# Performance work log

Hardware: AMD Instinct MI355X
Metric: run time of the kernel (lower is better)

## Reference

```python
import jax, jax.numpy as jnp
import numpy as np

K = 3
KK = K * K
PAD = 1          # kernel_size // 2
MAX_SHIFT = 8.0  # bias_range > 0
DEG = 2          # degrees = (2, 2), paon_type 'a'


def setup_inputs() -> dict:
    key = jax.random.key(0)
    ks = jax.random.split(key, 6)
    B, C, O, H, W = 4, 64, 64, 160, 160
    x = jax.random.normal(ks[0], (B, C, H, W), jnp.float32)
    # offset conv is 1x1: weight [2*K*K, C], bias [2*K*K]
    off_w = jax.random.normal(ks[1], (2 * KK, C), jnp.float32) * 0.1
    off_b = jax.random.normal(ks[2], (2 * KK,), jnp.float32) * 0.1
    scale = 1.0 / np.sqrt(C * KK).astype(np.float32)
    w_m = jax.random.normal(ks[3], (DEG * O, C, K, K), jnp.float32) * scale
    w_n = jax.random.normal(ks[4], (DEG * O, C, K, K), jnp.float32) * scale
    w0 = jax.random.normal(ks[5], (O,), jnp.float32) * 0.1
    return {"x": x, "off_w": off_w, "off_b": off_b, "w_m": w_m, "w_n": w_n, "w0": w0}


def _bilinear_sample(x, py, px):
    """x: [B,C,H,W]; py,px: [B,KK,H,W] -> [B,C,KK,H,W]; zero outside bounds."""
    B, C, H, W = x.shape
    xf = x.reshape(B, C, H * W)
    y0 = jnp.floor(py)
    x0 = jnp.floor(px)
    wy = py - y0
    wx = px - x0
    y0i = y0.astype(jnp.int32)
    x0i = x0.astype(jnp.int32)
    out = jnp.zeros((B, C) + py.shape[1:], x.dtype)
    corners = ((0, 0, (1 - wy) * (1 - wx)), (0, 1, (1 - wy) * wx),
               (1, 0, wy * (1 - wx)), (1, 1, wy * wx))
    for dy, dx, wgt in corners:
        yy = y0i + dy
        xx = x0i + dx
        valid = (yy >= 0) & (yy < H) & (xx >= 0) & (xx < W)
        idx = jnp.clip(yy, 0, H - 1) * W + jnp.clip(xx, 0, W - 1)
        g = jax.vmap(lambda f, i: f[:, i])(xf, idx.reshape(B, -1))  # [B,C,KK*H*W]
        out = out + g.reshape(B, C, *py.shape[1:]) * (wgt * valid)[:, None]
    return out


def _after_poly_a(y, ch, o, take_abs):
    # channel reorder + groupwise sum, per PaLaBase.after_poly_a
    order = np.array([(k * ch) % (ch * o) + k // o for k in range(ch * o)])
    y = y[:, order].reshape(y.shape[0], ch, o, *y.shape[2:])
    return jnp.abs(y).sum(2) if take_abs else y.sum(2)


def reference(x, off_w, off_b, w_m, w_n, w0):
    B, C, H, W = x.shape
    O = w0.shape[0]
    # --- DeformOffset: 1x1 conv -> clamp to image -> tanh soft-limit ---
    off_r = jnp.einsum('bchw,oc->bohw', x, off_w) + off_b[None, :, None, None]
    gy = jnp.arange(H, dtype=x.dtype)[None, None, :, None]
    gx = jnp.arange(W, dtype=x.dtype)[None, None, None, :]
    oy = jnp.clip(off_r[:, 0::2], -gy, H - gy)  # [B,KK,H,W] (dy per kernel pos)
    ox = jnp.clip(off_r[:, 1::2], -gx, W - gx)  # [B,KK,H,W] (dx per kernel pos)
    soft = lambda o: jnp.where(jnp.abs(o) >= MAX_SHIFT,
                               MAX_SHIFT * jnp.tanh(o / MAX_SHIFT), o)
    oy, ox = soft(oy), soft(ox)
    # --- deformable sampling grid (stride=1, dilation=1, zero padding) ---
    kidx = jnp.arange(KK)
    kh = (kidx // K).astype(x.dtype)[None, :, None, None]
    kw = (kidx % K).astype(x.dtype)[None, :, None, None]
    base_y = (jnp.arange(H, dtype=x.dtype) - PAD)[None, None, :, None]
    base_x = (jnp.arange(W, dtype=x.dtype) - PAD)[None, None, None, :]
    py = base_y + kh + oy
    px = base_x + kw + ox
    samp = _bilinear_sample(x, py, px)  # [B,C,KK,H,W]
    # --- Pade numerator / denominator convs on the sampled tensor ---
    pm_raw = jnp.einsum('bckhw,ock->bohw', samp, w_m.reshape(DEG * O, C, KK))
    qn_raw = jnp.einsum('bckhw,ock->bohw', samp, w_n.reshape(DEG * O, C, KK))
    pm = _after_poly_a(pm_raw, O, DEG, take_abs=False)
    qn = _after_poly_a(qn_raw, O, DEG, take_abs=True)
    # prepare_for_div_a: (pm + w0, 1 + qn)
    return (pm + w0[None, :, None, None]) / (1.0 + qn)
```

## Files before the change

### kernel.cpp

```cpp
#include <hip/hip_runtime.h>
#include <hip/hip_bf16.h>
#include <hip/hip_fp16.h>

#define Hh 160
#define Ww 160
#define Cc 64
#define HWc 25600
#define Bb 4

typedef __attribute__((ext_vector_type(8))) short short8;
typedef __attribute__((ext_vector_type(4))) float f32x4;

__device__ __forceinline__ unsigned short f2bf(float f) {
  unsigned int u = __float_as_uint(f);
  unsigned int r = u + 0x7FFFu + ((u >> 16) & 1u);
  return (unsigned short)(r >> 16);
}
__device__ __forceinline__ float bflo(unsigned int u) {
  return __uint_as_float(u << 16);
}
__device__ __forceinline__ float bfhi(unsigned int u) {
  return __uint_as_float(u & 0xffff0000u);
}

__global__ __launch_bounds__(256) void k_prep(
    const float* __restrict__ x, const float* __restrict__ wm,
    const float* __restrict__ wn, const float* __restrict__ ow,
    unsigned short* __restrict__ xT, unsigned short* __restrict__ bf) {
  if (blockIdx.x < 1600) {
    __shared__ unsigned short s[64][65];
    int wg = blockIdx.x;
    int b = wg / 400;
    int pix0 = (wg % 400) * 64;
    int l = threadIdx.x & 63, wv = threadIdx.x >> 6;
    const float* xb = x + (size_t)b * Cc * HWc + pix0;
#pragma unroll
    for (int i = 0; i < 16; i++) {
      int c = i * 4 + wv;
      s[c][l] = f2bf(xb[(size_t)c * HWc + l]);
    }
    __syncthreads();
    int p = threadIdx.x >> 2, ck = threadIdx.x & 3;
    unsigned int w[8];
#pragma unroll
    for (int j = 0; j < 8; j++) {
      unsigned int a = s[ck * 16 + 2 * j][p];
      unsigned int bb = s[ck * 16 + 2 * j + 1][p];
      w[j] = a | (bb << 16);
    }
    unsigned short* dst = xT + ((size_t)(b * HWc + pix0 + p)) * 64 + ck * 16;
    ((uint4*)dst)[0] = make_uint4(w[0], w[1], w[2], w[3]);
    ((uint4*)dst)[1] = make_uint4(w[4], w[5], w[6], w[7]);
  } else {
    int i = (blockIdx.x - 1600) * 256 + threadIdx.x;
    if (i < 9 * 2 * 12 * 64 * 8) {
      int j2 = i & 7;
      int lane = (i >> 3) & 63;
      int ntck = i >> 9;
      int nt = ntck % 12;
      int ck = ntck / 12;
      int kk = ck >> 1;
      int chunk = ck & 1;
      int n = nt * 16 + (lane & 15);
      int c = chunk * 32 + (lane >> 4) * 8 + j2;
      float v;
      if (n < 64)
        v = wm[(n * 64 + c) * 9 + kk] + wm[((n + 64) * 64 + c) * 9 + kk];
      else
        v = wn[((n - 64) * 64 + c) * 9 + kk];
      bf[i] = f2bf(v);
    } else if (i < 9 * 2 * 12 * 64 * 8 + 2 * 2 * 64 * 8) {
      int j = i - 9 * 2 * 12 * 64 * 8;
      int j2 = j & 7;
      int lane = (j >> 3) & 63;
      int rest = j >> 9;
      int ntile = rest & 1;
      int chunk = rest >> 1;
      int n = ntile * 16 + (lane & 15);
      int c = chunk * 32 + (lane >> 4) * 8 + j2;
      bf[i] = (n < 18) ? f2bf(ow[n * 64 + c]) : (unsigned short)0;
    }
  }
}

__device__ __forceinline__ void gather2(const char* __restrict__ gbase, uint4 D,
                                        int chB, uint4& c00, uint4& c01,
                                        uint4& c10, uint4& c11, float& w00,
                                        float& w01, float& w10, float& w11) {
  int bb = D.x + chB;
  int dxB = (int)(D.y & 0xffffu);
  int dyB = (int)(D.y >> 16);
  c00 = *(const uint4*)(gbase + bb);
  c01 = *(const uint4*)(gbase + bb + dxB);
  c10 = *(const uint4*)(gbase + bb + dyB);
  c11 = *(const uint4*)(gbase + bb + (dxB + dyB));
  float2 wA = __half22float2(*(const __half2*)&D.z);
  float2 wB = __half22float2(*(const __half2*)&D.w);
  w00 = wA.x; w01 = wA.y; w10 = wB.x; w11 = wB.y;
}

__device__ __forceinline__ void combine_write(unsigned short* Arow,
                                              const uint4& c00, const uint4& c01,
                                              const uint4& c10, const uint4& c11,
                                              float w00, float w01, float w10,
                                              float w11) {
  const unsigned int* a = (const unsigned int*)&c00;
  const unsigned int* b = (const unsigned int*)&c01;
  const unsigned int* c = (const unsigned int*)&c10;
  const unsigned int* d = (const unsigned int*)&c11;
  unsigned int o[4];
#pragma unroll
  for (int j = 0; j < 4; j++) {
    float lo = bflo(a[j]) * w00 + bflo(b[j]) * w01 + bflo(c[j]) * w10 +
               bflo(d[j]) * w11;
    float hi = bfhi(a[j]) * w00 + bfhi(b[j]) * w01 + bfhi(c[j]) * w10 +
               bfhi(d[j]) * w11;
    __hip_bfloat162 hh = __float22bfloat162_rn(make_float2(lo, hi));
    o[j] = *(unsigned int*)&hh;
  }
  *(uint4*)Arow = make_uint4(o[0], o[1], o[2], o[3]);
}

__global__ __launch_bounds__(256) void k_main(
    const unsigned short* __restrict__ xT, const float* __restrict__ w0,
    const float* __restrict__ off_b, const unsigned short* __restrict__ bfrag,
    const unsigned short* __restrict__ obfrag, float* __restrict__ out) {
  __shared__ unsigned short A[2][64 * 72];
  __shared__ uint4 gdesc[576];
  float2* spy = (float2*)&A[0][0];
  const int tid = threadIdx.x;
  const int wg = blockIdx.x;
  const int band = wg & 7;
  const int local = wg >> 3;
  const int b = local / 50;
  const int pix0 = band * 3200 + (local % 50) * 64;
  const int wv = tid >> 6;
  const int l = tid & 63;
  const int lm = l & 15;
  const int quad = l >> 4;
  const int ch8 = l & 7;
  const int pr = l >> 3;
  const int chB = ch8 * 16;

  const unsigned short* xTb = xT + (size_t)b * HWc * 64;
  const char* gbase = (const char*)xTb;

  f32x4 acc[3][4];
  const f32x4 zero = {0.f, 0.f, 0.f, 0.f};
#pragma unroll
  for (int j = 0; j < 3; j++)
#pragma unroll
    for (int pt = 0; pt < 4; pt++) acc[j][pt] = zero;

  {
    f32x4 aO0 = zero, aO1 = zero;
    const unsigned short* xrow = xTb + (size_t)(pix0 + wv * 16 + lm) * 64;
#pragma unroll
    for (int chunk = 0; chunk < 2; chunk++) {
      short8 sb = *(const short8*)(xrow + chunk * 32 + quad * 8);
      short8 wf0 = *(const short8*)&obfrag[((chunk * 2 + 0) * 64 + l) * 8];
      short8 wf1 = *(const short8*)&obfrag[((chunk * 2 + 1) * 64 + l) * 8];
      aO0 = __builtin_amdgcn_mfma_f32_16x16x32_bf16(wf0, sb, aO0, 0, 0, 0);
      aO1 = __builtin_amdgcn_mfma_f32_16x16x32_bf16(wf1, sb, aO1, 0, 0, 0);
    }
    int pix = pix0 + wv * 16 + lm;
    int h = pix / Ww, w = pix % Ww;
    float fh = (float)h, fw = (float)w;
#pragma unroll
    for (int rr = 0; rr < 2; rr++) {
      int n = quad * 4 + 2 * rr;
      int kk = n >> 1;
      float oy = aO0[2 * rr] + off_b[n];
      float ox = aO0[2 * rr + 1] + off_b[n + 1];
      oy = fminf(fmaxf(oy, -fh), 160.0f - fh);
      ox = fminf(fmaxf(ox, -fw), 160.0f - fw);
      if (fabsf(oy) >= 8.0f) oy = 8.0f * tanhf(oy * 0.125f);
      if (fabsf(ox) >= 8.0f) ox = 8.0f * tanhf(ox * 0.125f);
      spy[kk * 64 + wv * 16 + lm] =
          make_float2(fh - 1.0f + (float)(kk / 3) + oy,
                      fw - 1.0f + (float)(kk % 3) + ox);
    }
    if (quad == 0) {
      float oy = aO1[0] + off_b[16];
      float ox = aO1[1] + off_b[17];
      oy = fminf(fmaxf(oy, -fh), 160.0f - fh);
      ox = fminf(fmaxf(ox, -fw), 160.0f - fw);
      if (fabsf(oy) >= 8.0f) oy = 8.0f * tanhf(oy * 0.125f);
      if (fabsf(ox) >= 8.0f) ox = 8.0f * tanhf(ox * 0.125f);
      spy[8 * 64 + wv * 16 + lm] =
          make_float2(fh + 1.0f + oy, fw + 1.0f + ox);
    }
  }
  __syncthreads();

  for (int e = tid; e < 576; e += 256) {
    float2 P = spy[e];
    float py = P.x, pxv = P.y;
    float y0f = floorf(py), x0f = floorf(pxv);
    float wy = py - y0f, wx = pxv - x0f;
    int y0 = (int)y0f, x0 = (int)x0f;
    float vy0 = (y0 >= 0 && y0 < Hh) ? 1.f : 0.f;
    float vy1 = (y0 >= -1 && y0 < Hh - 1) ? 1.f : 0.f;
    float vx0 = (x0 >= 0 && x0 < Ww) ? 1.f : 0.f;
    float vx1 = (x0 >= -1 && x0 < Ww - 1) ? 1.f : 0.f;
    int r0 = min(max(y0, 0), Hh - 1);
    int r1 = min(max(y0 + 1, 0), Hh - 1);
    int c0 = min(max(x0, 0), Ww - 1);
    int c1 = min(max(x0 + 1, 0), Ww - 1);
    float w00 = (1.f - wy) * (1.f - wx) * vy0 * vx0;
    float w01 = (1.f - wy) * wx * vy0 * vx1;
    float w10 = wy * (1.f - wx) * vy1 * vx0;
    float w11 = wy * wx * vy1 * vx1;
    uint4 D;
    D.x = (unsigned int)((r0 * Ww + c0) * 128);
    D.y = (unsigned int)((c1 - c0) * 128) | ((unsigned int)((r1 - r0) * Ww * 128) << 16);
    __half2 hA = __floats2half2_rn(w00, w01);
    __half2 hB = __floats2half2_rn(w10, w11);
    D.z = *(unsigned int*)&hA;
    D.w = *(unsigned int*)&hB;
    gdesc[e] = D;
  }
  __syncthreads();

#pragma unroll
  for (int i = 0; i < 2; i++) {
    int pl = wv * 16 + i * 8 + pr;
    uint4 c00, c01, c10, c11;
    float w00, w01, w10, w11;
    gather2(gbase, gdesc[pl], chB, c00, c01, c10, c11, w00, w01, w10, w11);
    combine_write(&A[0][pl * 72 + ch8 * 8], c00, c01, c10, c11, w00, w01, w10,
                  w11);
  }
  __syncthreads();

  for (int kk = 0; kk < 9; kk++) {
    const int cur = kk & 1;
    uint4 g00[2], g01[2], g10[2], g11[2];
    float W00[2], W01[2], W10[2], W11[2];
    if (kk < 8) {
#pragma unroll
      for (int i = 0; i < 2; i++) {
        int pl = wv * 16 + i * 8 + pr;
        gather2(gbase, gdesc[(kk + 1) * 64 + pl], chB, g00[i], g01[i], g10[i],
                g11[i], W00[i], W01[i], W10[i], W11[i]);
      }
    }
#pragma unroll
    for (int chunk = 0; chunk < 2; chunk++) {
      short8 sfr[4];
#pragma unroll
      for (int pt = 0; pt < 4; pt++)
        sfr[pt] =
            *(const short8*)&A[cur][(pt * 16 + lm) * 72 + chunk * 32 + quad * 8];
      short8 wfr[3];
#pragma unroll
      for (int j = 0; j < 3; j++) {
        int nt = j * 4 + wv;
        wfr[j] = *(const short8*)&bfrag[((size_t)((kk * 2 + chunk) * 12 + nt) *
                                            64 + l) * 8];
      }
#pragma unroll
      for (int j = 0; j < 3; j++)
#pragma unroll
        for (int pt = 0; pt < 4; pt++)
          acc[j][pt] = __builtin_amdgcn_mfma_f32_16x16x32_bf16(
              wfr[j], sfr[pt], acc[j][pt], 0, 0, 0);
    }
    if (kk < 8) {
#pragma unroll
      for (int i = 0; i < 2; i++) {
        int pl = wv * 16 + i * 8 + pr;
        combine_write(&A[cur ^ 1][pl * 72 + ch8 * 8], g00[i], g01[i], g10[i],
                      g11[i], W00[i], W01[i], W10[i], W11[i]);
      }
    }
    __syncthreads();
  }

  float w0v[4];
#pragma unroll
  for (int r = 0; r < 4; r++) w0v[r] = w0[wv * 16 + quad * 4 + r];
  float* ob = out + (size_t)b * Cc * HWc + pix0;
#pragma unroll
  for (int pt = 0; pt < 4; pt++) {
#pragma unroll
    for (int r = 0; r < 4; r++) {
      int oc = wv * 16 + quad * 4 + r;
      float pm = acc[0][pt][r] + w0v[r];
      float qn = 1.0f + fabsf(acc[1][pt][r]) + fabsf(acc[2][pt][r]);
      ob[oc * HWc + pt * 16 + lm] = pm / qn;
    }
  }
}

extern "C" void kernel_launch(void* const* d_in, const int* in_sizes, int n_in,
                              void* d_out, int out_size, void* d_ws, size_t ws_size,
                              hipStream_t stream) {
  const float* x = (const float*)d_in[0];
  const float* off_w = (const float*)d_in[1];
  const float* off_b = (const float*)d_in[2];
  const float* w_m = (const float*)d_in[3];
  const float* w_n = (const float*)d_in[4];
  const float* w0 = (const float*)d_in[5];
  float* out = (float*)d_out;

  unsigned short* bfrag = (unsigned short*)d_ws;
  unsigned short* obfrag = (unsigned short*)((char*)d_ws + (size_t)221184);
  unsigned short* xT = (unsigned short*)((char*)d_ws + (size_t)225280);

  hipLaunchKernelGGL(k_prep, dim3(2040), dim3(256), 0, stream, x, w_m, w_n,
                     off_w, xT, bfrag);
  hipLaunchKernelGGL(k_main, dim3(1600), dim3(256), 0, stream, xT, w0, off_b,
                     bfrag, obfrag, out);
}
```

Before: 134.1 us.

## Widen prep transpose tiles, pad LDS stride, move combine before MFMA, set occupancy

The prep kernel now transposes 256 pixels per block using float4 loads and writes full 128-byte pixel rows, which cuts the block count and is meant to improve global load and store efficiency. In the main kernel the LDS row stride changes from 72 to 76 to alter bank mapping for the fragment reads. The gather-combine-write for the next kernel position now runs before the MFMAs rather than after them, which shortens register lifetimes but exposes the gather latency earlier. A launch-bounds occupancy hint of 4 is also added, which may constrain register allocation.

```diff
diff --git a/kernel.cpp b/kernel.cpp
--- a/kernel.cpp
+++ b/kernel.cpp
@@ -7,6 +7,7 @@
 #define Cc 64
 #define HWc 25600
 #define Bb 4
+#define AST 76
 
 typedef __attribute__((ext_vector_type(8))) short short8;
 typedef __attribute__((ext_vector_type(4))) float f32x4;
@@ -27,32 +28,36 @@
     const float* __restrict__ x, const float* __restrict__ wm,
     const float* __restrict__ wn, const float* __restrict__ ow,
     unsigned short* __restrict__ xT, unsigned short* __restrict__ bf) {
-  if (blockIdx.x < 1600) {
-    __shared__ unsigned short s[64][65];
+  if (blockIdx.x < 400) {
+    __shared__ unsigned short s[64][260];
     int wg = blockIdx.x;
-    int b = wg / 400;
-    int pix0 = (wg % 400) * 64;
+    int b = wg / 100;
+    int pix0 = (wg % 100) * 256;
     int l = threadIdx.x & 63, wv = threadIdx.x >> 6;
     const float* xb = x + (size_t)b * Cc * HWc + pix0;
 #pragma unroll
     for (int i = 0; i < 16; i++) {
       int c = i * 4 + wv;
-      s[c][l] = f2bf(xb[(size_t)c * HWc + l]);
+      float4 v = *(const float4*)&xb[(size_t)c * HWc + l * 4];
+      unsigned int d0 = (unsigned int)f2bf(v.x) | ((unsigned int)f2bf(v.y) << 16);
+      unsigned int d1 = (unsigned int)f2bf(v.z) | ((unsigned int)f2bf(v.w) << 16);
+      *(uint2*)&s[c][l * 4] = make_uint2(d0, d1);
     }
     __syncthreads();
-    int p = threadIdx.x >> 2, ck = threadIdx.x & 3;
-    unsigned int w[8];
-#pragma unroll
-    for (int j = 0; j < 8; j++) {
-      unsigned int a = s[ck * 16 + 2 * j][p];
-      unsigned int bb = s[ck * 16 + 2 * j + 1][p];
+    int p = threadIdx.x;
+    unsigned int w[32];
+#pragma unroll
+    for (int j = 0; j < 32; j++) {
+      unsigned int a = s[2 * j][p];
+      unsigned int bb = s[2 * j + 1][p];
       w[j] = a | (bb << 16);
     }
-    unsigned short* dst = xT + ((size_t)(b * HWc + pix0 + p)) * 64 + ck * 16;
-    ((uint4*)dst)[0] = make_uint4(w[0], w[1], w[2], w[3]);
-    ((uint4*)dst)[1] = make_uint4(w[4], w[5], w[6], w[7]);
+    unsigned short* dst = xT + ((size_t)(b * HWc + pix0 + p)) * 64;
+#pragma unroll
+    for (int j = 0; j < 8; j++)
+      ((uint4*)dst)[j] = make_uint4(w[4 * j], w[4 * j + 1], w[4 * j + 2], w[4 * j + 3]);
   } else {
-    int i = (blockIdx.x - 1600) * 256 + threadIdx.x;
+    int i = (blockIdx.x - 400) * 256 + threadIdx.x;
     if (i < 9 * 2 * 12 * 64 * 8) {
       int j2 = i & 7;
       int lane = (i >> 3) & 63;
@@ -121,11 +126,11 @@
   *(uint4*)Arow = make_uint4(o[0], o[1], o[2], o[3]);
 }
 
-__global__ __launch_bounds__(256) void k_main(
+__global__ __launch_bounds__(256, 4) void k_main(
     const unsigned short* __restrict__ xT, const float* __restrict__ w0,
     const float* __restrict__ off_b, const unsigned short* __restrict__ bfrag,
     const unsigned short* __restrict__ obfrag, float* __restrict__ out) {
-  __shared__ unsigned short A[2][64 * 72];
+  __shared__ unsigned short A[2][64 * AST];
   __shared__ uint4 gdesc[576];
   float2* spy = (float2*)&A[0][0];
   const int tid = threadIdx.x;
@@ -213,7 +218,8 @@
     float w11 = wy * wx * vy1 * vx1;
     uint4 D;
     D.x = (unsigned int)((r0 * Ww + c0) * 128);
-    D.y = (unsigned int)((c1 - c0) * 128) | ((unsigned int)((r1 - r0) * Ww * 128) << 16);
+    D.y = (unsigned int)((c1 - c0) * 128) |
+          ((unsigned int)((r1 - r0) * Ww * 128) << 16);
     __half2 hA = __floats2half2_rn(w00, w01);
     __half2 hB = __floats2half2_rn(w10, w11);
     D.z = *(unsigned int*)&hA;
@@ -228,30 +234,36 @@
     uint4 c00, c01, c10, c11;
     float w00, w01, w10, w11;
     gather2(gbase, gdesc[pl], chB, c00, c01, c10, c11, w00, w01, w10, w11);
-    combine_write(&A[0][pl * 72 + ch8 * 8], c00, c01, c10, c11, w00, w01, w10,
+    combine_write(&A[0][pl * AST + ch8 * 8], c00, c01, c10, c11, w00, w01, w10,
                   w11);
   }
   __syncthreads();
 
   for (int kk = 0; kk < 9; kk++) {
     const int cur = kk & 1;
-    uint4 g00[2], g01[2], g10[2], g11[2];
-    float W00[2], W01[2], W10[2], W11[2];
     if (kk < 8) {
+      uint4 g00[2], g01[2], g10[2], g11[2];
+      float W00[2], W01[2], W10[2], W11[2];
 #pragma unroll
       for (int i = 0; i < 2; i++) {
         int pl = wv * 16 + i * 8 + pr;
         gather2(gbase, gdesc[(kk + 1) * 64 + pl], chB, g00[i], g01[i], g10[i],
                 g11[i], W00[i], W01[i], W10[i], W11[i]);
       }
+#pragma unroll
+      for (int i = 0; i < 2; i++) {
+        int pl = wv * 16 + i * 8 + pr;
+        combine_write(&A[cur ^ 1][pl * AST + ch8 * 8], g00[i], g01[i], g10[i],
+                      g11[i], W00[i], W01[i], W10[i], W11[i]);
+      }
     }
 #pragma unroll
     for (int chunk = 0; chunk < 2; chunk++) {
       short8 sfr[4];
 #pragma unroll
       for (int pt = 0; pt < 4; pt++)
-        sfr[pt] =
-            *(const short8*)&A[cur][(pt * 16 + lm) * 72 + chunk * 32 + quad * 8];
+        sfr[pt] = *(const short8*)&A[cur][(pt * 16 + lm) * AST + chunk * 32 +
+                                          quad * 8];
       short8 wfr[3];
 #pragma unroll
       for (int j = 0; j < 3; j++) {
@@ -265,14 +277,6 @@
         for (int pt = 0; pt < 4; pt++)
           acc[j][pt] = __builtin_amdgcn_mfma_f32_16x16x32_bf16(
               wfr[j], sfr[pt], acc[j][pt], 0, 0, 0);
-    }
-    if (kk < 8) {
-#pragma unroll
-      for (int i = 0; i < 2; i++) {
-        int pl = wv * 16 + i * 8 + pr;
-        combine_write(&A[cur ^ 1][pl * 72 + ch8 * 8], g00[i], g01[i], g10[i],
-                      g11[i], W00[i], W01[i], W10[i], W11[i]);
-      }
     }
     __syncthreads();
   }
@@ -308,7 +312,7 @@
   unsigned short* obfrag = (unsigned short*)((char*)d_ws + (size_t)221184);
   unsigned short* xT = (unsigned short*)((char*)d_ws + (size_t)225280);
 
-  hipLaunchKernelGGL(k_prep, dim3(2040), dim3(256), 0, stream, x, w_m, w_n,
+  hipLaunchKernelGGL(k_prep, dim3(840), dim3(256), 0, stream, x, w_m, w_n,
                      off_w, xT, bfrag);
   hipLaunchKernelGGL(k_main, dim3(1600), dim3(256), 0, stream, xT, w0, off_b,
                      bfrag, obfrag, out);
```

Result: no change. 133.6 us (-0.4%).
